# Kernel optimization log

Measured on AMD Instinct MI355X. Metric: run time of the kernel, lower is better.

## Reference

```python
import jax, jax.numpy as jnp
import numpy as np

B, C, H, W = 8, 512, 64, 64
HEADS, GROUPS, EPS = 4, 32, 1e-5


def setup_inputs() -> dict:
    key = jax.random.key(0)
    ks = jax.random.split(key, 7)
    s = 0.02
    return {
        "x": jax.random.normal(ks[0], (B, C, H, W), dtype=jnp.float32),
        "gn_w": jnp.ones((C,), dtype=jnp.float32),
        "gn_b": jnp.zeros((C,), dtype=jnp.float32),
        "qkv_w": jax.random.normal(ks[1], (3 * C, C), dtype=jnp.float32) * s,
        "qkv_b": jnp.zeros((3 * C,), dtype=jnp.float32),
        "proj_w": jax.random.normal(ks[2], (C, C), dtype=jnp.float32) * s,
        "proj_b": jnp.zeros((C,), dtype=jnp.float32),
    }


def reference(x, gn_w, gn_b, qkv_w, qkv_b, proj_w, proj_b):
    b, c, h, w = x.shape
    d = c // HEADS  # per-head channel dim
    n = h * w
    # GroupNorm(32, C)
    xg = x.reshape(b, GROUPS, -1)
    mu = xg.mean(axis=-1, keepdims=True)
    var = xg.var(axis=-1, keepdims=True)
    hn = ((xg - mu) * jax.lax.rsqrt(var + EPS)).reshape(b, c, h, w)
    hn = hn * gn_w[:, None, None] + gn_b[:, None, None]
    # 1x1 conv qkv: [3C, C] contraction over channels
    qkv = jnp.einsum('oc,bchw->bohw', qkv_w, hn) + qkv_b[:, None, None]
    qkv = qkv.reshape(b, 3, HEADS, d, n)
    q, k, v = qkv[:, 0], qkv[:, 1], qkv[:, 2]  # each [b, heads, d, n]
    # NOTE: as in the source, q @ k^T contracts over spatial dim -> [b,heads,d,d]
    attn = jnp.einsum('bhdn,bhen->bhde', q, k) * (d ** -0.5)
    attn = jax.nn.softmax(attn, axis=-1)
    out = jnp.einsum('bhde,bhen->bhdn', attn, v).reshape(b, c, h, w)
    out = jnp.einsum('oc,bchw->bohw', proj_w, out) + proj_b[:, None, None]
    return x + out
```

## Files before the change

kernel.cpp:

```cpp
#include <hip/hip_runtime.h>
#include <hip/hip_bf16.h>

typedef __hip_bfloat16 bf16;
typedef __bf16 v8bf __attribute__((ext_vector_type(8)));
typedef float  v4f  __attribute__((ext_vector_type(4)));

struct __align__(8) bf16x4 { bf16 x, y, z, w; };

__device__ __forceinline__ bf16 f2b(float v) { return __float2bfloat16(v); }

#define NSP 4096
#define CCH 512

__device__ __forceinline__ void async_cp16(const bf16* g, __bf16* l) {
    __builtin_amdgcn_global_load_lds(
        (const __attribute__((address_space(1))) unsigned int*)(unsigned long long)g,
        (__attribute__((address_space(3))) unsigned int*)(unsigned int)(unsigned long long)l,
        16, 0, 0);
}

__global__ __launch_bounds__(256) void wconv_kernel(const float* __restrict__ src,
                                                    bf16* __restrict__ dst, int n4) {
    int i = blockIdx.x * 256 + threadIdx.x;
    if (i < n4) {
        float4 v = ((const float4*)src)[i];
        bf16x4 o = { f2b(v.x), f2b(v.y), f2b(v.z), f2b(v.w) };
        ((bf16x4*)dst)[i] = o;
    }
}

__global__ __launch_bounds__(256) void gn_stats_kernel(const float* __restrict__ x,
                                                       float* __restrict__ stats) {
    int blk = blockIdx.x;
    int b = blk >> 5, g = blk & 31;
    size_t base = ((size_t)(b * CCH + g * 16)) * NSP;
    const float4* xp4 = (const float4*)(x + base);
    int t = threadIdx.x;
    float s = 0.f, s2 = 0.f;
    for (int i = t; i < 16384; i += 256) {
        float4 v = xp4[i];
        s  += v.x + v.y + v.z + v.w;
        s2 += v.x * v.x + v.y * v.y + v.z * v.z + v.w * v.w;
    }
    for (int off = 32; off > 0; off >>= 1) {
        s  += __shfl_down(s, off);
        s2 += __shfl_down(s2, off);
    }
    __shared__ float red[8];
    int wid = t >> 6, lid = t & 63;
    if (lid == 0) { red[wid] = s; red[wid + 4] = s2; }
    __syncthreads();
    if (t == 0) {
        float ts  = red[0] + red[1] + red[2] + red[3];
        float ts2 = red[4] + red[5] + red[6] + red[7];
        float mean = ts * (1.f / 65536.f);
        float var  = ts2 * (1.f / 65536.f) - mean * mean;
        stats[blk * 2]     = mean;
        stats[blk * 2 + 1] = rsqrtf(var + 1e-5f);
    }
}

__global__ __launch_bounds__(256) void gn_norm_t_kernel(const float* __restrict__ x,
                                                        const float* __restrict__ gw,
                                                        const float* __restrict__ gb,
                                                        const float* __restrict__ stats,
                                                        bf16* __restrict__ hnT) {
    __shared__ float sT[64][65];
    int n0 = blockIdx.x * 64, c0 = blockIdx.y * 64, b = blockIdx.z;
    int t = threadIdx.x;
    int cl = t >> 4, nl4 = (t & 15) << 2;
#pragma unroll
    for (int it = 0; it < 4; ++it) {
        int crow = cl + it * 16;
        int c = c0 + crow;
        int bg = b * 32 + (c >> 4);
        float mean = stats[bg * 2], rstd = stats[bg * 2 + 1];
        float wsc = gw[c] * rstd;
        float bb  = gb[c] - mean * wsc;
        float4 v = *(const float4*)&x[((long)b * CCH + c) * NSP + n0 + nl4];
        sT[crow][nl4 + 0] = v.x * wsc + bb;
        sT[crow][nl4 + 1] = v.y * wsc + bb;
        sT[crow][nl4 + 2] = v.z * wsc + bb;
        sT[crow][nl4 + 3] = v.w * wsc + bb;
    }
    __syncthreads();
    int nl = t >> 4, cl4 = (t & 15) << 2;
#pragma unroll
    for (int it = 0; it < 4; ++it) {
        int nrow = nl + it * 16;
        bf16x4 ov = { f2b(sT[cl4 + 0][nrow]), f2b(sT[cl4 + 1][nrow]),
                      f2b(sT[cl4 + 2][nrow]), f2b(sT[cl4 + 3][nrow]) };
        *(bf16x4*)&hnT[((long)b * NSP + n0 + nrow) * CCH + c0 + cl4] = ov;
    }
}

__device__ __forceinline__ void gemm_core(const bf16* __restrict__ A, long as,
                                          const bf16* __restrict__ B, long bs,
                                          int K, v4f acc[4][4],
                                          __bf16* sA, __bf16* sB) {
    int t = threadIdx.x;
    int lane = t & 63, wv = t >> 6;
    int wr = wv >> 1, wc = wv & 1;
    int lq = lane & 15, quad = lane >> 4;
    const __bf16* aBase = sA + (wr * 64) * 64;
    const __bf16* bBase = sB + (wc * 64) * 64;

    for (int k0 = 0; k0 < K; k0 += 64) {
        __syncthreads();
#pragma unroll
        for (int i = 0; i < 4; ++i) {
            int idx = i * 256 + t;
            int row = idx >> 3;
            int ko  = (idx & 7) * 8;
            async_cp16(A + (long)row * as + k0 + ko, sA + idx * 8);
            async_cp16(B + (long)row * bs + k0 + ko, sB + idx * 8);
        }
        __syncthreads();
#pragma unroll
        for (int kk = 0; kk < 2; ++kk) {
            v8bf a[4], bfr[4];
#pragma unroll
            for (int i = 0; i < 4; ++i)
                a[i] = *(const v8bf*)(aBase + (i * 16 + lq) * 64 + kk * 32 + quad * 8);
#pragma unroll
            for (int j = 0; j < 4; ++j)
                bfr[j] = *(const v8bf*)(bBase + (j * 16 + lq) * 64 + kk * 32 + quad * 8);
#pragma unroll
            for (int i = 0; i < 4; ++i)
#pragma unroll
                for (int j = 0; j < 4; ++j)
                    acc[i][j] = __builtin_amdgcn_mfma_f32_16x16x32_bf16(a[i], bfr[j], acc[i][j], 0, 0, 0);
        }
    }
}

__global__ __launch_bounds__(256) void qkv_gemm_kernel(const bf16* __restrict__ hnT,
                                                       const bf16* __restrict__ qkv_wb,
                                                       const float* __restrict__ qkv_b,
                                                       bf16* __restrict__ qkbuf,
                                                       bf16* __restrict__ vT) {
    __shared__ __align__(16) __bf16 sA[128 * 64];
    __shared__ __align__(16) __bf16 sB[128 * 64];
    int n0 = blockIdx.x * 128, o0 = blockIdx.y * 128, b = blockIdx.z;
    int t = threadIdx.x, lane = t & 63, wv = t >> 6, wr = wv >> 1, wc = wv & 1;
    int lq = lane & 15, quad = lane >> 4;
    v4f acc[4][4];
#pragma unroll
    for (int j = 0; j < 4; ++j) {
        float bias = qkv_b[o0 + wc * 64 + j * 16 + lq];
#pragma unroll
        for (int i = 0; i < 4; ++i) acc[i][j] = { bias, bias, bias, bias };
    }
    gemm_core(hnT + ((long)b * NSP + n0) * CCH, CCH,
              qkv_wb + (long)o0 * CCH, CCH, CCH, acc, sA, sB);
#pragma unroll
    for (int j = 0; j < 4; ++j) {
        int o = o0 + wc * 64 + j * 16 + lq;
#pragma unroll
        for (int i = 0; i < 4; ++i) {
            int n = n0 + wr * 64 + i * 16 + quad * 4;
            v4f v = acc[i][j];
            if (o0 < 1024) {
                bf16x4 ov = { f2b(v[0]), f2b(v[1]), f2b(v[2]), f2b(v[3]) };
                *(bf16x4*)&qkbuf[((long)b * 1024 + o) * NSP + n] = ov;
            } else {
#pragma unroll
                for (int r = 0; r < 4; ++r)
                    vT[((long)b * NSP + n + r) * CCH + (o - 1024)] = f2b(v[r]);
            }
        }
    }
}

__global__ __launch_bounds__(256) void qk_gemm_kernel(const bf16* __restrict__ qkbuf,
                                                      float* __restrict__ P_part) {
    __shared__ __align__(16) __bf16 sA[128 * 64];
    __shared__ __align__(16) __bf16 sB[128 * 64];
    int s = blockIdx.x, bh = blockIdx.y;
    int b = bh >> 2, h = bh & 3;
    const bf16* q  = qkbuf + ((long)b * 1024 + h * 128) * NSP + s * 512;
    const bf16* kk = qkbuf + ((long)b * 1024 + 512 + h * 128) * NSP + s * 512;
    v4f acc[4][4] = {};
    gemm_core(q, NSP, kk, NSP, 512, acc, sA, sB);
    float* Pp = P_part + ((long)s * 32 + bh) * 16384;
    int t = threadIdx.x, lane = t & 63, wv = t >> 6, wr = wv >> 1, wc = wv & 1;
    int lq = lane & 15, quad = lane >> 4;
#pragma unroll
    for (int j = 0; j < 4; ++j) {
        int e = wc * 64 + j * 16 + lq;
#pragma unroll
        for (int i = 0; i < 4; ++i) {
            int d = wr * 64 + i * 16 + quad * 4;
            v4f v = acc[i][j];
#pragma unroll
            for (int r = 0; r < 4; ++r) Pp[(long)(d + r) * 128 + e] = v[r];
        }
    }
}

__global__ __launch_bounds__(128) void softmax_kernel(const float* __restrict__ P_part,
                                                      bf16* __restrict__ Pb) {
    int row = blockIdx.x;
    int bh = row >> 7, d = row & 127;
    int t = threadIdx.x;
    float v = 0.f;
#pragma unroll
    for (int s = 0; s < 8; ++s)
        v += P_part[((long)s * 32 + bh) * 16384 + (long)d * 128 + t];
    v *= 0.08838834764831845f;
    float m = v;
    for (int off = 32; off > 0; off >>= 1) m = fmaxf(m, __shfl_down(m, off));
    __shared__ float sm[2];
    if ((t & 63) == 0) sm[t >> 6] = m;
    __syncthreads();
    m = fmaxf(sm[0], sm[1]);
    float e = __expf(v - m);
    float ssum = e;
    for (int off = 32; off > 0; off >>= 1) ssum += __shfl_down(ssum, off);
    __shared__ float ss[2];
    if ((t & 63) == 0) ss[t >> 6] = ssum;
    __syncthreads();
    ssum = ss[0] + ss[1];
    Pb[(long)row * 128 + t] = f2b(e / ssum);
}

__global__ __launch_bounds__(256) void pv_gemm_kernel(const bf16* __restrict__ Pb,
                                                      const bf16* __restrict__ vT,
                                                      bf16* __restrict__ attT) {
    __shared__ __align__(16) __bf16 sA[128 * 64];
    __shared__ __align__(16) __bf16 sB[128 * 64];
    int n0 = blockIdx.x * 128, bh = blockIdx.y;
    int b = bh >> 2, h = bh & 3;
    v4f acc[4][4] = {};
    gemm_core(Pb + (long)bh * 16384, 128,
              vT + ((long)b * NSP + n0) * CCH + h * 128, CCH, 128, acc, sA, sB);
    int t = threadIdx.x, lane = t & 63, wv = t >> 6, wr = wv >> 1, wc = wv & 1;
    int lq = lane & 15, quad = lane >> 4;
#pragma unroll
    for (int j = 0; j < 4; ++j) {
        int n = n0 + wc * 64 + j * 16 + lq;
#pragma unroll
        for (int i = 0; i < 4; ++i) {
            int d = wr * 64 + i * 16 + quad * 4;
            v4f v = acc[i][j];
            bf16x4 ov = { f2b(v[0]), f2b(v[1]), f2b(v[2]), f2b(v[3]) };
            *(bf16x4*)&attT[((long)b * NSP + n) * CCH + h * 128 + d] = ov;
        }
    }
}

__global__ __launch_bounds__(256) void proj_gemm_kernel(const bf16* __restrict__ attT,
                                                        const bf16* __restrict__ proj_wb,
                                                        const float* __restrict__ proj_b,
                                                        const float* __restrict__ x,
                                                        float* __restrict__ out) {
    __shared__ __align__(16) __bf16 sA[128 * 64];
    __shared__ __align__(16) __bf16 sB[128 * 64];
    int n0 = blockIdx.x * 128, c0 = blockIdx.y * 128, b = blockIdx.z;
    int t = threadIdx.x, lane = t & 63, wv = t >> 6, wr = wv >> 1, wc = wv & 1;
    int lq = lane & 15, quad = lane >> 4;
    v4f acc[4][4];
#pragma unroll
    for (int j = 0; j < 4; ++j) {
        int c = c0 + wc * 64 + j * 16 + lq;
        float bias = proj_b[c];
#pragma unroll
        for (int i = 0; i < 4; ++i) {
            int n = n0 + wr * 64 + i * 16 + quad * 4;
            float4 r = *(const float4*)&x[((long)b * CCH + c) * NSP + n];
            acc[i][j] = { r.x + bias, r.y + bias, r.z + bias, r.w + bias };
        }
    }
    gemm_core(attT + ((long)b * NSP + n0) * CCH, CCH,
              proj_wb + (long)c0 * CCH, CCH, CCH, acc, sA, sB);
#pragma unroll
    for (int j = 0; j < 4; ++j) {
        int c = c0 + wc * 64 + j * 16 + lq;
#pragma unroll
        for (int i = 0; i < 4; ++i) {
            int n = n0 + wr * 64 + i * 16 + quad * 4;
            long idx = ((long)b * CCH + c) * NSP + n;
            v4f v = acc[i][j];
            float4 ov = { v[0], v[1], v[2], v[3] };
            *(float4*)&out[idx] = ov;
        }
    }
}

extern "C" void kernel_launch(void* const* d_in, const int* in_sizes, int n_in,
                              void* d_out, int out_size, void* d_ws, size_t ws_size,
                              hipStream_t stream) {
    const float* x      = (const float*)d_in[0];
    const float* gn_w   = (const float*)d_in[1];
    const float* gn_b   = (const float*)d_in[2];
    const float* qkv_w  = (const float*)d_in[3];
    const float* qkv_b  = (const float*)d_in[4];
    const float* proj_w = (const float*)d_in[5];
    const float* proj_b = (const float*)d_in[6];
    float* out = (float*)d_out;

    char* ws = (char*)d_ws;
    bf16*  hnT    = (bf16*)ws;
    float* P_part = (float*)ws;
    bf16*  attT   = (bf16*)ws;
    bf16*  qkbuf  = (bf16*)(ws + 33554432);
    bf16*  vT     = (bf16*)(ws + 100663296);
    bf16*  Pb     = (bf16*)(ws + 134217728);
    float* stats  = (float*)(ws + 135266304);
    bf16*  qkv_wb = (bf16*)(ws + 135270400);
    bf16*  proj_wb= (bf16*)(ws + 136843264);

    wconv_kernel<<<768, 256, 0, stream>>>(qkv_w, qkv_wb, 196608);
    wconv_kernel<<<256, 256, 0, stream>>>(proj_w, proj_wb, 65536);
    gn_stats_kernel<<<256, 256, 0, stream>>>(x, stats);
    gn_norm_t_kernel<<<dim3(64, 8, 8), 256, 0, stream>>>(x, gn_w, gn_b, stats, hnT);
    qkv_gemm_kernel<<<dim3(32, 12, 8), 256, 0, stream>>>(hnT, qkv_wb, qkv_b, qkbuf, vT);
    qk_gemm_kernel<<<dim3(8, 32), 256, 0, stream>>>(qkbuf, P_part);
    softmax_kernel<<<4096, 128, 0, stream>>>(P_part, Pb);
    pv_gemm_kernel<<<dim3(32, 32), 256, 0, stream>>>(Pb, vT, attT);
    proj_gemm_kernel<<<dim3(32, 4, 8), 256, 0, stream>>>(attT, proj_wb, proj_b, x, out);
}
```

Measured before the change: 334.6 us.

## Halve GEMM K-tile and swizzle LDS layout to avoid bank conflicts

The shared GEMM core now stages 32-wide K slices instead of 64, so LDS buffers shrink from 128x64 to 128x32 per operand. The global-to-LDS copy uses an XOR-like column rotation, and fragment reads apply the matching swizzle to reduce LDS bank conflicts. Smaller LDS footprint may allow more resident blocks per CU. The cost is twice as many K iterations, each with two barriers and no double buffering, so synchronisation overhead per MFMA doubles.

Measured after the change: 330.8 us. No clear change (-1.1%).

```diff
diff --git a/kernel.cpp b/kernel.cpp
--- a/kernel.cpp
+++ b/kernel.cpp
@@ -102,35 +102,36 @@
     int lane = t & 63, wv = t >> 6;
     int wr = wv >> 1, wc = wv & 1;
     int lq = lane & 15, quad = lane >> 4;
-    const __bf16* aBase = sA + (wr * 64) * 64;
-    const __bf16* bBase = sB + (wc * 64) * 64;
-
-    for (int k0 = 0; k0 < K; k0 += 64) {
+    int p0 = t, p1 = t + 256;
+    int r0 = p0 >> 2, c0 = ((p0 & 3) - ((p0 >> 3) & 3)) & 3;
+    int r1 = p1 >> 2, c1 = ((p1 & 3) - ((p1 >> 3) & 3)) & 3;
+    __bf16* lA0 = sA + p0 * 8;
+    __bf16* lA1 = sA + p1 * 8;
+    __bf16* lB0 = sB + p0 * 8;
+    __bf16* lB1 = sB + p1 * 8;
+    int ssw = (quad + ((lq >> 1) & 3)) & 3;
+    const __bf16* aBase = sA + (wr * 64) * 32 + ssw * 8;
+    const __bf16* bBase = sB + (wc * 64) * 32 + ssw * 8;
+
+    for (int k0 = 0; k0 < K; k0 += 32) {
         __syncthreads();
-#pragma unroll
-        for (int i = 0; i < 4; ++i) {
-            int idx = i * 256 + t;
-            int row = idx >> 3;
-            int ko  = (idx & 7) * 8;
-            async_cp16(A + (long)row * as + k0 + ko, sA + idx * 8);
-            async_cp16(B + (long)row * bs + k0 + ko, sB + idx * 8);
-        }
+        async_cp16(A + (long)r0 * as + k0 + c0 * 8, lA0);
+        async_cp16(A + (long)r1 * as + k0 + c1 * 8, lA1);
+        async_cp16(B + (long)r0 * bs + k0 + c0 * 8, lB0);
+        async_cp16(B + (long)r1 * bs + k0 + c1 * 8, lB1);
         __syncthreads();
-#pragma unroll
-        for (int kk = 0; kk < 2; ++kk) {
-            v8bf a[4], bfr[4];
-#pragma unroll
-            for (int i = 0; i < 4; ++i)
-                a[i] = *(const v8bf*)(aBase + (i * 16 + lq) * 64 + kk * 32 + quad * 8);
+        v8bf a[4], bfr[4];
+#pragma unroll
+        for (int i = 0; i < 4; ++i)
+            a[i] = *(const v8bf*)(aBase + (i * 16 + lq) * 32);
+#pragma unroll
+        for (int j = 0; j < 4; ++j)
+            bfr[j] = *(const v8bf*)(bBase + (j * 16 + lq) * 32);
+#pragma unroll
+        for (int i = 0; i < 4; ++i)
 #pragma unroll
             for (int j = 0; j < 4; ++j)
-                bfr[j] = *(const v8bf*)(bBase + (j * 16 + lq) * 64 + kk * 32 + quad * 8);
-#pragma unroll
-            for (int i = 0; i < 4; ++i)
-#pragma unroll
-                for (int j = 0; j < 4; ++j)
-                    acc[i][j] = __builtin_amdgcn_mfma_f32_16x16x32_bf16(a[i], bfr[j], acc[i][j], 0, 0, 0);
-        }
+                acc[i][j] = __builtin_amdgcn_mfma_f32_16x16x32_bf16(a[i], bfr[j], acc[i][j], 0, 0, 0);
     }
 }
 
@@ -139,8 +140,8 @@
                                                        const float* __restrict__ qkv_b,
                                                        bf16* __restrict__ qkbuf,
                                                        bf16* __restrict__ vT) {
-    __shared__ __align__(16) __bf16 sA[128 * 64];
-    __shared__ __align__(16) __bf16 sB[128 * 64];
+    __shared__ __align__(16) __bf16 sA[128 * 32];
+    __shared__ __align__(16) __bf16 sB[128 * 32];
     int n0 = blockIdx.x * 128, o0 = blockIdx.y * 128, b = blockIdx.z;
     int t = threadIdx.x, lane = t & 63, wv = t >> 6, wr = wv >> 1, wc = wv & 1;
     int lq = lane & 15, quad = lane >> 4;
@@ -174,8 +175,8 @@
 
 __global__ __launch_bounds__(256) void qk_gemm_kernel(const bf16* __restrict__ qkbuf,
                                                       float* __restrict__ P_part) {
-    __shared__ __align__(16) __bf16 sA[128 * 64];
-    __shared__ __align__(16) __bf16 sB[128 * 64];
+    __shared__ __align__(16) __bf16 sA[128 * 32];
+    __shared__ __align__(16) __bf16 sB[128 * 32];
     int s = blockIdx.x, bh = blockIdx.y;
     int b = bh >> 2, h = bh & 3;
     const bf16* q  = qkbuf + ((long)b * 1024 + h * 128) * NSP + s * 512;
@@ -227,8 +228,8 @@
 __global__ __launch_bounds__(256) void pv_gemm_kernel(const bf16* __restrict__ Pb,
                                                       const bf16* __restrict__ vT,
                                                       bf16* __restrict__ attT) {
-    __shared__ __align__(16) __bf16 sA[128 * 64];
-    __shared__ __align__(16) __bf16 sB[128 * 64];
+    __shared__ __align__(16) __bf16 sA[128 * 32];
+    __shared__ __align__(16) __bf16 sB[128 * 32];
     int n0 = blockIdx.x * 128, bh = blockIdx.y;
     int b = bh >> 2, h = bh & 3;
     v4f acc[4][4] = {};
@@ -254,8 +255,8 @@
                                                         const float* __restrict__ proj_b,
                                                         const float* __restrict__ x,
                                                         float* __restrict__ out) {
-    __shared__ __align__(16) __bf16 sA[128 * 64];
-    __shared__ __align__(16) __bf16 sB[128 * 64];
+    __shared__ __align__(16) __bf16 sA[128 * 32];
+    __shared__ __align__(16) __bf16 sB[128 * 32];
     int n0 = blockIdx.x * 128, c0 = blockIdx.y * 128, b = blockIdx.z;
     int t = threadIdx.x, lane = t & 63, wv = t >> 6, wr = wv >> 1, wc = wv & 1;
     int lq = lane & 15, quad = lane >> 4;
```
